# Kernel optimization log

Hardware: AMD Instinct MI355X
Metric: run time of the kernel (lower is better)

Reference implementation:

```python
import jax, jax.numpy as jnp
import numpy as np

H = 1024
L = 4

def _lstm_layer(xs, w_ih, w_hh, b):
    # xs: [B, T, in]; w_ih: [4H, in]; w_hh: [4H, H]; b: [4H] (b_ih + b_hh)
    xp = jnp.einsum('bti,gi->btg', xs, w_ih) + b  # [B, T, 4H]
    xp = jnp.swapaxes(xp, 0, 1)                   # [T, B, 4H]
    B = xs.shape[0]
    h0 = jnp.zeros((B, H), xs.dtype)
    c0 = jnp.zeros((B, H), xs.dtype)

    def step(carry, xp_t):
        h, c = carry
        gates = xp_t + h @ w_hh.T                 # [B, 4H]
        i, f, g, o = jnp.split(gates, 4, axis=-1)  # PyTorch gate order i,f,g,o
        i = jax.nn.sigmoid(i)
        f = jax.nn.sigmoid(f)
        g = jnp.tanh(g)
        o = jax.nn.sigmoid(o)
        c = f * c + i * g
        h = o * jnp.tanh(c)
        return (h, c), h

    (hT, cT), hs = jax.lax.scan(step, (h0, c0), xp)
    return jnp.swapaxes(hs, 0, 1), hT             # [B, T, H], [B, H]


def setup_inputs() -> dict:
    key = jax.random.key(0)
    ks = jax.random.split(key, 8)
    s = 1.0 / np.sqrt(H)
    u = lambda k, shp: jax.random.uniform(k, shp, jnp.float32, -s, s)
    return {
        'x': jax.random.normal(ks[0], (64, 256, 2), jnp.float32),
        'w_ih0': u(ks[1], (4 * H, 2)),            # layer 0 input weights
        'w_ih_rest': u(ks[2], (L - 1, 4 * H, H)), # layers 1..3 input weights
        'w_hh': u(ks[3], (L, 4 * H, H)),
        'b_ih': u(ks[4], (L, 4 * H)),
        'b_hh': u(ks[5], (L, 4 * H)),
        'fc_w': u(ks[6], (1, H)),
        'fc_b': u(ks[7], (1,)),
    }


def reference(x, w_ih0, w_ih_rest, w_hh, b_ih, b_hh, fc_w, fc_b):
    # 4-layer LSTM, batch_first, zero initial states; dropout inactive (eval mode).
    hs, hT = _lstm_layer(x, w_ih0, w_hh[0], b_ih[0] + b_hh[0])
    for l in range(1, L):
        hs, hT = _lstm_layer(hs, w_ih_rest[l - 1], w_hh[l], b_ih[l] + b_hh[l])
    # fc applied to final hidden state of last layer
    return hT @ fc_w.T + fc_b                      # [B, 1]
```

## Files before the change

kernel.cpp:

```cpp
#include <hip/hip_runtime.h>
#include <hip/hip_bf16.h>
#include <hip/hip_fp16.h>


#define H      1024
#define BATCH  64
#define T      256
#define RINGN  8

typedef _Float16 f16x8 __attribute__((ext_vector_type(8)));
typedef _Float16 f16x4 __attribute__((ext_vector_type(4)));
typedef float    f32x4 __attribute__((ext_vector_type(4)));

#define WPACK_HH_SZ  (4ull*64*32*4*64*8*2)
#define WPACK_IH_SZ  (3ull*64*32*4*64*8*2)
#define HRING_OFF    (WPACK_HH_SZ + WPACK_IH_SZ)
#define SLOT_ELEMS   65536
#define SLOT_BYTES   131072ull
#define CNT_INTS     (4*257*16)
#define CNT_BYTES    ((unsigned long long)CNT_INTS*4)

__host__ __device__ __forceinline__ unsigned long long ring_bytes(int nslot) {
  return 4ull*(unsigned)nslot*SLOT_BYTES;
}
__device__ __forceinline__ int cidx(int l, int s) { return (l*257 + s)*16; }
__device__ __forceinline__ int fidx(int l, int w) { return (l*64 + w)*16; }

__device__ __forceinline__ int aslot(int s, int fresh) {
  if (!fresh) return s & 7;
  return (s >= 256) ? 256 : (int)(__brev((unsigned)s) >> 24);
}

__device__ __forceinline__ void wait_eq64(int* p) {
  int it = 0;
  while (__hip_atomic_load(p, __ATOMIC_RELAXED, __HIP_MEMORY_SCOPE_AGENT) < 64) {
    __builtin_amdgcn_s_sleep(1);
    if (++it > 100000000) break;
  }
}

__device__ __forceinline__ void wait_ge(const int* p, int tgt) {
  int it = 0;
  while (__hip_atomic_load(p, __ATOMIC_RELAXED, __HIP_MEMORY_SCOPE_AGENT) < tgt) {
    __builtin_amdgcn_s_sleep(1);
    if (++it > 100000000) break;
  }
}

__device__ __forceinline__ f16x8 load_h8_sc(const _Float16* p) {
  const unsigned long long* q = (const unsigned long long*)p;
  unsigned long long lo = __hip_atomic_load(q,     __ATOMIC_RELAXED, __HIP_MEMORY_SCOPE_AGENT);
  unsigned long long hi = __hip_atomic_load(q + 1, __ATOMIC_RELAXED, __HIP_MEMORY_SCOPE_AGENT);
  union { unsigned long long u[2]; f16x8 v; } c;
  c.u[0] = lo; c.u[1] = hi;
  return c.v;
}

__global__ void pack_kernel(const float* __restrict__ w_ih_rest,
                            const float* __restrict__ w_hh,
                            char* __restrict__ ws, int nslot)
{
  const long long NS_HH = 4ll*64*32*4*64;
  const long long NS_IH = 3ll*64*32*4*64;
  const long long NS_HZ = 4ll*8192;
  const long long NTOT  = NS_HH + NS_IH + NS_HZ + 256;
  _Float16* whh_dst = (_Float16*)ws;
  _Float16* wih_dst = (_Float16*)(ws + WPACK_HH_SZ);
  int* cnt = (int*)(ws + HRING_OFF + ring_bytes(nslot));
  for (long long i = blockIdx.x*(long long)blockDim.x + threadIdx.x; i < NTOT;
       i += (long long)gridDim.x*blockDim.x) {
    if (i < NS_HH + NS_IH) {
      const bool is_hh = (i < NS_HH);
      long long slot = is_hh ? i : (i - NS_HH);
      long long j = slot;
      int lane = (int)(j & 63); j >>= 6;
      int nt   = (int)(j & 3);  j >>= 2;
      int ks   = (int)(j & 31); j >>= 5;
      int wg   = (int)(j & 63); j >>= 6;
      int l    = (int)j;
      int row = nt*1024 + wg*16 + (lane & 15);
      int col = ks*32 + (lane >> 4)*8;
      const float* src = (is_hh ? w_hh : w_ih_rest) + ((long long)l*4096 + row)*1024 + col;
      f16x8 v;
      #pragma unroll
      for (int e = 0; e < 8; e++) v[e] = (_Float16)src[e];
      *(f16x8*)((is_hh ? whh_dst : wih_dst) + slot*8) = v;
    } else if (i < NS_HH + NS_IH + NS_HZ) {
      long long j = i - (NS_HH + NS_IH);
      long long l = j >> 13;
      long long off = j & 8191;
      uint4 z = make_uint4(0,0,0,0);
      ((uint4*)(ws + HRING_OFF))[(l*(long long)nslot)*8192 + off] = z;
    } else {
      int k = (int)(i - (NS_HH + NS_IH + NS_HZ));
      cnt[k*16] = 0;
    }
  }
}

__global__ __launch_bounds__(256, 1) void lstm_main(
    const float* __restrict__ x,
    const float* __restrict__ wih0,
    const float* __restrict__ bih,
    const float* __restrict__ bhh,
    char* __restrict__ ws, int nslot, int fresh)
{
  __builtin_amdgcn_fence(__ATOMIC_ACQUIRE, "agent");

  extern __shared__ char lds[];
  _Float16* whh_lds = (_Float16*)lds;
  _Float16* buf0    = (_Float16*)(lds + 131072);
  _Float16* buf1    = (_Float16*)(lds + 139264);

  const int l   = blockIdx.x >> 6;
  const int wg  = blockIdx.x & 63;
  const int tid = threadIdx.x;
  const int wave = tid >> 6;
  const int lane = tid & 63;

  const _Float16* wpack_hh = (const _Float16*)ws + (size_t)(l*64 + wg)*65536;
  const _Float16* wpack_ih = (l > 0)
      ? (const _Float16*)(ws + WPACK_HH_SZ) + (size_t)((l-1)*64 + wg)*65536
      : wpack_hh;
  _Float16* hring = (_Float16*)(ws + HRING_OFF);
  int* cnt  = (int*)(ws + HRING_OFF + ring_bytes(nslot));
  int* cnt2 = cnt + CNT_INTS;

  {
    const uint4* src = (const uint4*)wpack_hh;
    uint4* dst = (uint4*)whh_lds;
    for (int i = tid; i < 8192; i += 256) dst[i] = src[i];
  }

  const int b_ew = tid >> 2;
  const int u0   = (tid & 3) * 4;
  float cst[4] = {0.f, 0.f, 0.f, 0.f};
  float bias[4][4];
  float wx0[4][4], wx1[4][4];
  #pragma unroll
  for (int ii = 0; ii < 4; ii++) {
    #pragma unroll
    for (int g = 0; g < 4; g++) {
      int row = g*1024 + wg*16 + u0 + ii;
      bias[ii][g] = bih[l*4096 + row] + bhh[l*4096 + row];
      if (l == 0) { wx0[ii][g] = wih0[row*2]; wx1[ii][g] = wih0[row*2 + 1]; }
      else        { wx0[ii][g] = 0.f;         wx1[ii][g] = 0.f; }
    }
  }
  __syncthreads();

  const int m_row = lane & 15, quad = lane >> 4;

  for (int s = 1; s <= T; s++) {
    if (fresh) {
      if (l == 0) {
        if (lane < 16) wait_ge(cnt + fidx(0, wave*16 + lane), s - 1);
      } else {
        if (wave == 0)      { if (lane < 32) wait_ge(cnt + fidx(l-1, lane),      s); }
        else if (wave == 1) { if (lane < 32) wait_ge(cnt + fidx(l-1, 32 + lane), s); }
        else if (wave == 2) { if (lane < 32) wait_ge(cnt + fidx(l,   lane),      s - 1); }
        else                { if (lane < 32) wait_ge(cnt + fidx(l,   32 + lane), s - 1); }
      }
    } else {
      if (wave == 0) {
        wait_ge(cnt + fidx(l, lane), s - 1);
      } else if (wave == 1) {
        if (l > 0) wait_ge(cnt + fidx(l - 1, lane), s);
      } else if (tid == 128) {
        if (l < 3 && s > RINGN) wait_eq64(&cnt2[cidx(l, s-RINGN)]);
      }
      __syncthreads();
    }

    const _Float16* asrc = (l > 0 && wave < 2)
        ? hring + ((size_t)(l-1)*nslot + aslot(s,   fresh))*SLOT_ELEMS
        : hring + ((size_t)l*nslot     + aslot(s-1, fresh))*SLOT_ELEMS;

    f32x4 acc[4][4];
    #pragma unroll
    for (int mt = 0; mt < 4; mt++)
      #pragma unroll
      for (int nt = 0; nt < 4; nt++) acc[mt][nt] = (f32x4){0.f, 0.f, 0.f, 0.f};

    auto kbody = [&](int ks, bool from_lds, bool plain) {
      const int kb = ks*32 + quad*8;
      f16x8 a[4], bb[4];
      #pragma unroll
      for (int mt = 0; mt < 4; mt++) {
        const _Float16* ap = asrc + (size_t)(mt*16 + m_row)*1024 + kb;
        a[mt] = plain ? *(const f16x8*)ap : load_h8_sc(ap);
      }
      if (from_lds) {
        #pragma unroll
        for (int nt = 0; nt < 4; nt++)
          bb[nt] = *(const f16x8*)(whh_lds + ((ks*4 + nt)*64 + lane)*8);
      } else {
        #pragma unroll
        for (int nt = 0; nt < 4; nt++)
          bb[nt] = *(const f16x8*)(wpack_ih + ((size_t)(ks*4 + nt)*64 + lane)*8);
      }
      #pragma unroll
      for (int mt = 0; mt < 4; mt++)
        #pragma unroll
        for (int nt = 0; nt < 4; nt++)
          acc[mt][nt] = __builtin_amdgcn_mfma_f32_16x16x32_f16(a[mt], bb[nt], acc[mt][nt], 0, 0, 0);
    };

    if (fresh) {
      if (l == 0) {
        #pragma unroll 4
        for (int i = 0; i < 8; i++) kbody(wave*8 + i, true, true);
      } else if (wave < 2) {
        #pragma unroll 4
        for (int i = 0; i < 16; i++) kbody(wave*16 + i, false, true);
      } else {
        #pragma unroll 4
        for (int i = 0; i < 16; i++) kbody((wave-2)*16 + i, true, true);
      }
    } else {
      if (l == 0) {
        #pragma unroll 2
        for (int i = 0; i < 8; i++) kbody(wave*8 + i, true, false);
      } else if (wave < 2) {
        #pragma unroll 2
        for (int i = 0; i < 16; i++) kbody(wave*16 + i, false, false);
      } else {
        #pragma unroll 2
        for (int i = 0; i < 16; i++) kbody((wave-2)*16 + i, true, false);
      }
    }

    _Float16* mybuf = ((wave & 1) == 0) ? buf0 : buf1;
    if (wave >= 2) {
      #pragma unroll
      for (int mt = 0; mt < 4; mt++)
        #pragma unroll
        for (int nt = 0; nt < 4; nt++) {
          f16x4 v;
          #pragma unroll
          for (int e = 0; e < 4; e++) v[e] = (_Float16)acc[mt][nt][e];
          *(f16x4*)(mybuf + ((mt*4 + nt)*64 + lane)*4) = v;
        }
    }
    __syncthreads();
    if (wave < 2) {
      #pragma unroll
      for (int mt = 0; mt < 4; mt++)
        #pragma unroll
        for (int nt = 0; nt < 4; nt++) {
          f16x4 p = *(f16x4*)(mybuf + ((mt*4 + nt)*64 + lane)*4);
          f16x4 v;
          #pragma unroll
          for (int e = 0; e < 4; e++) v[e] = (_Float16)(acc[mt][nt][e] + (float)p[e]);
          *(f16x4*)(mybuf + ((mt*4 + nt)*64 + lane)*4) = v;
        }
    }
    if (!fresh && tid == 0 && l > 0)
      __hip_atomic_fetch_add(&cnt2[cidx(l-1, s)], 1, __ATOMIC_RELAXED, __HIP_MEMORY_SCOPE_AGENT);
    __syncthreads();

    {
      const int mt = b_ew >> 4, q = (b_ew & 15) >> 2, reg = b_ew & 3;
      float xs0 = 0.f, xs1 = 0.f;
      if (l == 0) {
        xs0 = x[((size_t)b_ew*T + (s-1))*2];
        xs1 = x[((size_t)b_ew*T + (s-1))*2 + 1];
      }
      f16x4 hv;
      #pragma unroll
      for (int ii = 0; ii < 4; ii++) {
        const int u = u0 + ii;
        float pre[4];
        #pragma unroll
        for (int g = 0; g < 4; g++) {
          int idx = ((mt*4 + g)*64 + (u + 16*q))*4 + reg;
          pre[g] = (float)buf0[idx] + (float)buf1[idx] + bias[ii][g]
                 + wx0[ii][g]*xs0 + wx1[ii][g]*xs1;
        }
        float ig = 1.f/(1.f + __expf(-pre[0]));
        float fg = 1.f/(1.f + __expf(-pre[1]));
        float gg = 2.f/(1.f + __expf(-2.f*pre[2])) - 1.f;
        float og = 1.f/(1.f + __expf(-pre[3]));
        float c  = fg*cst[ii] + ig*gg;
        cst[ii] = c;
        float th = 2.f/(1.f + __expf(-2.f*c)) - 1.f;
        hv[ii] = (_Float16)(og*th);
      }
      _Float16* hdst = hring + ((size_t)l*nslot + aslot(s, fresh))*SLOT_ELEMS
                     + (size_t)b_ew*1024 + wg*16 + u0;
      union { f16x4 v; unsigned long long u; } cv; cv.v = hv;
      __hip_atomic_store((unsigned long long*)hdst, cv.u,
                         __ATOMIC_RELAXED, __HIP_MEMORY_SCOPE_AGENT);
    }
    __syncthreads();
    if (tid == 0)
      __hip_atomic_store(cnt + fidx(l, wg), s,
                         __ATOMIC_RELAXED, __HIP_MEMORY_SCOPE_AGENT);
  }
}

__global__ void fc_kernel(const char* __restrict__ ws,
                          const float* __restrict__ fcw,
                          const float* __restrict__ fcb,
                          float* __restrict__ out, int nslot, int fresh)
{
  const _Float16* h3 = (const _Float16*)(ws + HRING_OFF)
                     + ((size_t)3*nslot + aslot(T, fresh))*SLOT_ELEMS;
  __shared__ float red[256];
  const int tid = threadIdx.x;
  const int b = tid >> 2, p = tid & 3;
  float sum = 0.f;
  for (int j = p*256; j < p*256 + 256; j++)
    sum += fcw[j] * (float)h3[(size_t)b*1024 + j];
  red[tid] = sum;
  __syncthreads();
  if (p == 0)
    out[b] = red[tid] + red[tid+1] + red[tid+2] + red[tid+3] + fcb[0];
}

extern "C" void kernel_launch(void* const* d_in, const int* in_sizes, int n_in,
                              void* d_out, int out_size, void* d_ws, size_t ws_size,
                              hipStream_t stream)
{
  const float* x    = (const float*)d_in[0];
  const float* wih0 = (const float*)d_in[1];
  const float* wihr = (const float*)d_in[2];
  const float* whh  = (const float*)d_in[3];
  const float* bih  = (const float*)d_in[4];
  const float* bhh  = (const float*)d_in[5];
  const float* fcw  = (const float*)d_in[6];
  const float* fcb  = (const float*)d_in[7];
  float* out = (float*)d_out;
  char* ws = (char*)d_ws;
  (void)in_sizes; (void)n_in; (void)out_size;

  const unsigned long long ws_big   = HRING_OFF + ring_bytes(257) + 2*CNT_BYTES;
  const unsigned long long ws_small = HRING_OFF + ring_bytes(8)   + 2*CNT_BYTES;
  if (ws_size < ws_small) return;
  const int fresh = (ws_size >= ws_big) ? 1 : 0;
  const int nslot = fresh ? 257 : 8;

  hipFuncSetAttribute(reinterpret_cast<const void*>(lstm_main),
                      hipFuncAttributeMaxDynamicSharedMemorySize, 147456);

  hipMemsetAsync(ws + HRING_OFF + ring_bytes(nslot), 0, (size_t)(2*CNT_BYTES), stream);
  pack_kernel<<<512, 256, 0, stream>>>(wihr, whh, ws, nslot);
  lstm_main<<<256, 256, 147456, stream>>>(x, wih0, bih, bhh, ws, nslot, fresh);
  fc_kernel<<<1, 256, 0, stream>>>(ws, fcw, fcb, out, nslot, fresh);
}
```

Baseline: 3.800 ms.

## Use four per-wave partial buffers and drop the intermediate reduction barrier

Each wave now writes its partial gate sums to its own LDS buffer, and the elementwise stage sums all four. This removes one __syncthreads and the read-modify-write pass that folded wave pairs together. To make room for the larger buffers, only 28 of the 32 W_hh k-slices are cached in LDS and the last four are read from global memory. The k-range split across waves is rebalanced to match, which adds global weight traffic on the recurrent critical path.

After: 3.423 ms. 1.11x faster.

```diff
diff --git a/kernel.cpp b/kernel.cpp
--- a/kernel.cpp
+++ b/kernel.cpp
@@ -109,8 +109,7 @@
 
   extern __shared__ char lds[];
   _Float16* whh_lds = (_Float16*)lds;
-  _Float16* buf0    = (_Float16*)(lds + 131072);
-  _Float16* buf1    = (_Float16*)(lds + 139264);
+  _Float16* bufs    = (_Float16*)(lds + 114688);
 
   const int l   = blockIdx.x >> 6;
   const int wg  = blockIdx.x & 63;
@@ -129,7 +128,7 @@
   {
     const uint4* src = (const uint4*)wpack_hh;
     uint4* dst = (uint4*)whh_lds;
-    for (int i = tid; i < 8192; i += 256) dst[i] = src[i];
+    for (int i = tid; i < 7168; i += 256) dst[i] = src[i];
   }
 
   const int b_ew = tid >> 2;
@@ -182,7 +181,7 @@
       #pragma unroll
       for (int nt = 0; nt < 4; nt++) acc[mt][nt] = (f32x4){0.f, 0.f, 0.f, 0.f};
 
-    auto kbody = [&](int ks, bool from_lds, bool plain) {
+    auto kb_lds = [&](int ks, bool plain) {
       const int kb = ks*32 + quad*8;
       f16x8 a[4], bb[4];
       #pragma unroll
@@ -190,48 +189,59 @@
         const _Float16* ap = asrc + (size_t)(mt*16 + m_row)*1024 + kb;
         a[mt] = plain ? *(const f16x8*)ap : load_h8_sc(ap);
       }
-      if (from_lds) {
-        #pragma unroll
-        for (int nt = 0; nt < 4; nt++)
-          bb[nt] = *(const f16x8*)(whh_lds + ((ks*4 + nt)*64 + lane)*8);
-      } else {
-        #pragma unroll
-        for (int nt = 0; nt < 4; nt++)
-          bb[nt] = *(const f16x8*)(wpack_ih + ((size_t)(ks*4 + nt)*64 + lane)*8);
-      }
+      #pragma unroll
+      for (int nt = 0; nt < 4; nt++)
+        bb[nt] = *(const f16x8*)(whh_lds + ((ks*4 + nt)*64 + lane)*8);
       #pragma unroll
       for (int mt = 0; mt < 4; mt++)
         #pragma unroll
         for (int nt = 0; nt < 4; nt++)
           acc[mt][nt] = __builtin_amdgcn_mfma_f32_16x16x32_f16(a[mt], bb[nt], acc[mt][nt], 0, 0, 0);
     };
-
-    if (fresh) {
-      if (l == 0) {
+    auto kb_glob = [&](int ks, const _Float16* bsrc, bool plain) {
+      const int kb = ks*32 + quad*8;
+      f16x8 a[4], bb[4];
+      #pragma unroll
+      for (int mt = 0; mt < 4; mt++) {
+        const _Float16* ap = asrc + (size_t)(mt*16 + m_row)*1024 + kb;
+        a[mt] = plain ? *(const f16x8*)ap : load_h8_sc(ap);
+      }
+      #pragma unroll
+      for (int nt = 0; nt < 4; nt++)
+        bb[nt] = *(const f16x8*)(bsrc + ((size_t)(ks*4 + nt)*64 + lane)*8);
+      #pragma unroll
+      for (int mt = 0; mt < 4; mt++)
+        #pragma unroll
+        for (int nt = 0; nt < 4; nt++)
+          acc[mt][nt] = __builtin_amdgcn_mfma_f32_16x16x32_f16(a[mt], bb[nt], acc[mt][nt], 0, 0, 0);
+    };
+
+    const bool pl = (fresh != 0);
+    if (l == 0) {
+      if (wave < 3) {
         #pragma unroll 4
-        for (int i = 0; i < 8; i++) kbody(wave*8 + i, true, true);
-      } else if (wave < 2) {
-        #pragma unroll 4
-        for (int i = 0; i < 16; i++) kbody(wave*16 + i, false, true);
+        for (int i = 0; i < 8; i++) kb_lds(wave*8 + i, pl);
       } else {
         #pragma unroll 4
-        for (int i = 0; i < 16; i++) kbody((wave-2)*16 + i, true, true);
-      }
+        for (int i = 0; i < 4; i++) kb_lds(24 + i, pl);
+        #pragma unroll
+        for (int i = 0; i < 4; i++) kb_glob(28 + i, wpack_hh, pl);
+      }
+    } else if (wave < 2) {
+      #pragma unroll 4
+      for (int i = 0; i < 16; i++) kb_glob(wave*16 + i, wpack_ih, pl);
+    } else if (wave == 2) {
+      #pragma unroll 4
+      for (int i = 0; i < 16; i++) kb_lds(i, pl);
     } else {
-      if (l == 0) {
-        #pragma unroll 2
-        for (int i = 0; i < 8; i++) kbody(wave*8 + i, true, false);
-      } else if (wave < 2) {
-        #pragma unroll 2
-        for (int i = 0; i < 16; i++) kbody(wave*16 + i, false, false);
-      } else {
-        #pragma unroll 2
-        for (int i = 0; i < 16; i++) kbody((wave-2)*16 + i, true, false);
-      }
-    }
-
-    _Float16* mybuf = ((wave & 1) == 0) ? buf0 : buf1;
-    if (wave >= 2) {
+      #pragma unroll 4
+      for (int i = 0; i < 12; i++) kb_lds(16 + i, pl);
+      #pragma unroll
+      for (int i = 0; i < 4; i++) kb_glob(28 + i, wpack_hh, pl);
+    }
+
+    {
+      _Float16* mybuf = bufs + (size_t)wave*4096;
       #pragma unroll
       for (int mt = 0; mt < 4; mt++)
         #pragma unroll
@@ -242,19 +252,6 @@
           *(f16x4*)(mybuf + ((mt*4 + nt)*64 + lane)*4) = v;
         }
     }
-    __syncthreads();
-    if (wave < 2) {
-      #pragma unroll
-      for (int mt = 0; mt < 4; mt++)
-        #pragma unroll
-        for (int nt = 0; nt < 4; nt++) {
-          f16x4 p = *(f16x4*)(mybuf + ((mt*4 + nt)*64 + lane)*4);
-          f16x4 v;
-          #pragma unroll
-          for (int e = 0; e < 4; e++) v[e] = (_Float16)(acc[mt][nt][e] + (float)p[e]);
-          *(f16x4*)(mybuf + ((mt*4 + nt)*64 + lane)*4) = v;
-        }
-    }
     if (!fresh && tid == 0 && l > 0)
       __hip_atomic_fetch_add(&cnt2[cidx(l-1, s)], 1, __ATOMIC_RELAXED, __HIP_MEMORY_SCOPE_AGENT);
     __syncthreads();
@@ -274,8 +271,9 @@
         #pragma unroll
         for (int g = 0; g < 4; g++) {
           int idx = ((mt*4 + g)*64 + (u + 16*q))*4 + reg;
-          pre[g] = (float)buf0[idx] + (float)buf1[idx] + bias[ii][g]
-                 + wx0[ii][g]*xs0 + wx1[ii][g]*xs1;
+          pre[g] = (float)bufs[idx] + (float)bufs[4096 + idx]
+                 + (float)bufs[8192 + idx] + (float)bufs[12288 + idx]
+                 + bias[ii][g] + wx0[ii][g]*xs0 + wx1[ii][g]*xs1;
         }
         float ig = 1.f/(1.f + __expf(-pre[0]));
         float fg = 1.f/(1.f + __expf(-pre[1]));
```
